# Kernel tuning notes

Measured on AMD Instinct MI355X. Metric: run time of the kernel, lower is better.

Reference implementation:

```python
import jax, jax.numpy as jnp
import numpy as np

B, DZ, DS, DH = 8192, 1024, 64, 4096

def setup_inputs() -> dict:
    key = jax.random.key(0)
    ks = jax.random.split(key, 8)
    r1 = 1.0 / np.sqrt(DZ)   # W1 init range (last dim dz)
    r2 = 1.0 / np.sqrt(DH)   # W2 init range (last dim dim_hidden)
    rc = 1.0 / np.sqrt(DS)   # C init range
    return {
        "z": jax.random.normal(ks[0], (B, DZ), jnp.float32),
        "s": jax.random.normal(ks[1], (B, DS), jnp.float32),
        "A": jnp.full((DZ,), 0.95, jnp.float32),
        "W1": jax.random.uniform(ks[2], (DH, DZ), jnp.float32, -r1, r1),
        "W2": jax.random.uniform(ks[3], (DZ, DH), jnp.float32, -r2, r2),
        "h1": jax.random.normal(ks[4], (DH,), jnp.float32),
        "h2": jax.random.normal(ks[5], (DZ,), jnp.float32),
        "C": jax.random.uniform(ks[6], (DZ, DS), jnp.float32, -rc, rc),
    }

def reference(z, s, A, W1, W2, h1, h2, C):
    # PLRNN step, W_trial=False, mean_center=False, noise=0:
    # z' = A*z + relu(z @ W1.T + h1) @ W2.T + h2 + s @ C.T
    z_activated = jax.nn.relu(z @ W1.T + h1)          # [B, DH]
    return A * z + z_activated @ W2.T + h2 + s @ C.T  # [B, DZ]
```

## Files before the change

kernel.cpp:

```cpp
#include <hip/hip_runtime.h>

#define BB 8192
#define DZ 1024
#define DS 64
#define DH 4096
#define KEXT (DH + DS)

typedef float floatx4 __attribute__((ext_vector_type(4)));
typedef __bf16 bf16x8 __attribute__((ext_vector_type(8)));
typedef __attribute__((address_space(1))) void* as1_void_ptr;
typedef __attribute__((address_space(3))) void* as3_void_ptr;

__device__ __forceinline__ void async_copy16(const void* g, void* l) {
    __builtin_amdgcn_global_load_lds((as1_void_ptr)g, (as3_void_ptr)l, 16, 0, 0);
}


__global__ void cvt_f32_bf16(const float* __restrict__ in, __bf16* __restrict__ out, int n4) {
    int i = blockIdx.x * blockDim.x + threadIdx.x;
    if (i < n4) {
        float4 v = ((const float4*)in)[i];
        __bf16* o = out + (size_t)i * 4;
        o[0] = (__bf16)v.x; o[1] = (__bf16)v.y; o[2] = (__bf16)v.z; o[3] = (__bf16)v.w;
    }
}

__global__ void build_B2(const float* __restrict__ W2, const float* __restrict__ C,
                         __bf16* __restrict__ B2b) {
    int j = blockIdx.x;
    for (int h = threadIdx.x; h < KEXT; h += 256) {
        float v = (h < DH) ? W2[(size_t)j * DH + h] : C[(size_t)j * DS + (h - DH)];
        B2b[(size_t)j * KEXT + h] = (__bf16)v;
    }
}

__global__ void stage_s(const float* __restrict__ s, __bf16* __restrict__ Hb) {
    int idx = blockIdx.x * 256 + threadIdx.x;
    int b = idx >> 6, k = idx & 63;
    Hb[(size_t)b * KEXT + DH + k] = (__bf16)s[idx];
}


__global__ __launch_bounds__(256) void gemm1_relu(
    const __bf16* __restrict__ Ag, const __bf16* __restrict__ Bg,
    const float* __restrict__ h1, __bf16* __restrict__ Hb)
{
    constexpr int K = DZ, ldA = DZ, ldB = DZ;
    __shared__ __align__(16) __bf16 As[128 * 32];
    __shared__ __align__(16) __bf16 Bs[128 * 32];

    const int tid = threadIdx.x;
    const int wave = tid >> 6, lane = tid & 63;
    const int wm = wave >> 1, wn = wave & 1;
    const int row0 = blockIdx.x * 128;
    const int col0 = blockIdx.y * 128;

    const __bf16* a0 = Ag + (size_t)(row0 + (tid >> 2)) * ldA + (tid & 3) * 8;
    const __bf16* b0 = Bg + (size_t)(col0 + (tid >> 2)) * ldB + (tid & 3) * 8;
    __bf16* lA = As + wave * 512;
    __bf16* lB = Bs + wave * 512;

    const __bf16* Afrag = As + (wm * 64 + (lane & 15)) * 32 + (lane >> 4) * 8;
    const __bf16* Bfrag = Bs + (wn * 64 + (lane & 15)) * 32 + (lane >> 4) * 8;

    floatx4 acc[4][4];
#pragma unroll
    for (int i = 0; i < 4; ++i)
#pragma unroll
        for (int j = 0; j < 4; ++j) acc[i][j] = (floatx4)0.0f;

    for (int kt = 0; kt < K / 32; ++kt) {
        const __bf16* ak = a0 + kt * 32;
        const __bf16* bk = b0 + kt * 32;
        async_copy16(ak,            lA);
        async_copy16(ak + 64 * ldA, lA + 2048);
        async_copy16(bk,            lB);
        async_copy16(bk + 64 * ldB, lB + 2048);
        __builtin_amdgcn_s_waitcnt(0);
        __syncthreads();

        bf16x8 af[4], bfr[4];
#pragma unroll
        for (int i = 0; i < 4; ++i) af[i] = *(const bf16x8*)(Afrag + i * 16 * 32);
#pragma unroll
        for (int j = 0; j < 4; ++j) bfr[j] = *(const bf16x8*)(Bfrag + j * 16 * 32);
#pragma unroll
        for (int i = 0; i < 4; ++i)
#pragma unroll
            for (int j = 0; j < 4; ++j)
                acc[i][j] = __builtin_amdgcn_mfma_f32_16x16x32_bf16(af[i], bfr[j], acc[i][j], 0, 0, 0);
        __syncthreads();
    }

    const int r0 = row0 + wm * 64 + (lane >> 4) * 4;
    const int c0 = col0 + wn * 64 + (lane & 15);
#pragma unroll
    for (int i = 0; i < 4; ++i) {
#pragma unroll
        for (int j = 0; j < 4; ++j) {
            int c = c0 + j * 16;
            float bias = h1[c];
#pragma unroll
            for (int rg = 0; rg < 4; ++rg) {
                int r = r0 + i * 16 + rg;
                float v = acc[i][j][rg] + bias;
                v = v > 0.0f ? v : 0.0f;
                Hb[(size_t)r * KEXT + c] = (__bf16)v;
            }
        }
    }
}


__global__ __launch_bounds__(256) void gemm2_out(
    const __bf16* __restrict__ Ag, const __bf16* __restrict__ Bg,
    const float* __restrict__ Adiag, const float* __restrict__ h2,
    const float* __restrict__ zf, float* __restrict__ out)
{
    constexpr int K = KEXT, ldA = KEXT, ldB = KEXT;
    __shared__ __align__(16) __bf16 As[128 * 32];
    __shared__ __align__(16) __bf16 Bs[128 * 32];

    const int tid = threadIdx.x;
    const int wave = tid >> 6, lane = tid & 63;
    const int wm = wave >> 1, wn = wave & 1;
    const int row0 = blockIdx.x * 128;
    const int col0 = blockIdx.y * 128;

    const __bf16* a0 = Ag + (size_t)(row0 + (tid >> 2)) * ldA + (tid & 3) * 8;
    const __bf16* b0 = Bg + (size_t)(col0 + (tid >> 2)) * ldB + (tid & 3) * 8;
    __bf16* lA = As + wave * 512;
    __bf16* lB = Bs + wave * 512;

    const __bf16* Afrag = As + (wm * 64 + (lane & 15)) * 32 + (lane >> 4) * 8;
    const __bf16* Bfrag = Bs + (wn * 64 + (lane & 15)) * 32 + (lane >> 4) * 8;

    floatx4 acc[4][4];
#pragma unroll
    for (int i = 0; i < 4; ++i)
#pragma unroll
        for (int j = 0; j < 4; ++j) acc[i][j] = (floatx4)0.0f;

    for (int kt = 0; kt < K / 32; ++kt) {
        const __bf16* ak = a0 + kt * 32;
        const __bf16* bk = b0 + kt * 32;
        async_copy16(ak,            lA);
        async_copy16(ak + 64 * ldA, lA + 2048);
        async_copy16(bk,            lB);
        async_copy16(bk + 64 * ldB, lB + 2048);
        __builtin_amdgcn_s_waitcnt(0);
        __syncthreads();

        bf16x8 af[4], bfr[4];
#pragma unroll
        for (int i = 0; i < 4; ++i) af[i] = *(const bf16x8*)(Afrag + i * 16 * 32);
#pragma unroll
        for (int j = 0; j < 4; ++j) bfr[j] = *(const bf16x8*)(Bfrag + j * 16 * 32);
#pragma unroll
        for (int i = 0; i < 4; ++i)
#pragma unroll
            for (int j = 0; j < 4; ++j)
                acc[i][j] = __builtin_amdgcn_mfma_f32_16x16x32_bf16(af[i], bfr[j], acc[i][j], 0, 0, 0);
        __syncthreads();
    }

    const int r0 = row0 + wm * 64 + (lane >> 4) * 4;
    const int c0 = col0 + wn * 64 + (lane & 15);
#pragma unroll
    for (int i = 0; i < 4; ++i) {
#pragma unroll
        for (int j = 0; j < 4; ++j) {
            int c = c0 + j * 16;
            float aj = Adiag[c];
            float hj = h2[c];
#pragma unroll
            for (int rg = 0; rg < 4; ++rg) {
                int r = r0 + i * 16 + rg;
                out[(size_t)r * DZ + c] = acc[i][j][rg] + aj * zf[(size_t)r * DZ + c] + hj;
            }
        }
    }
}


extern "C" void kernel_launch(void* const* d_in, const int* in_sizes, int n_in,
                              void* d_out, int out_size, void* d_ws, size_t ws_size,
                              hipStream_t stream) {
    const float* z  = (const float*)d_in[0];
    const float* s  = (const float*)d_in[1];
    const float* A  = (const float*)d_in[2];
    const float* W1 = (const float*)d_in[3];
    const float* W2 = (const float*)d_in[4];
    const float* h1 = (const float*)d_in[5];
    const float* h2 = (const float*)d_in[6];
    const float* C  = (const float*)d_in[7];
    float* out = (float*)d_out;

    char* ws = (char*)d_ws;
    size_t offHb  = 0;
    size_t offZb  = offHb  + (size_t)BB * KEXT * 2;
    size_t offW1b = offZb  + (size_t)BB * DZ * 2;
    size_t offB2b = offW1b + (size_t)DH * DZ * 2;
    __bf16* Hb  = (__bf16*)(ws + offHb);
    __bf16* zb  = (__bf16*)(ws + offZb);
    __bf16* W1b = (__bf16*)(ws + offW1b);
    __bf16* B2b = (__bf16*)(ws + offB2b);

    cvt_f32_bf16<<<(BB * DZ / 4 + 255) / 256, 256, 0, stream>>>(z, zb, BB * DZ / 4);
    cvt_f32_bf16<<<(DH * DZ / 4 + 255) / 256, 256, 0, stream>>>(W1, W1b, DH * DZ / 4);
    build_B2<<<DZ, 256, 0, stream>>>(W2, C, B2b);
    stage_s<<<BB * DS / 256, 256, 0, stream>>>(s, Hb);

    gemm1_relu<<<dim3(BB / 128, DH / 128), 256, 0, stream>>>(zb, W1b, h1, Hb);
    gemm2_out<<<dim3(BB / 128, DZ / 128), 256, 0, stream>>>(Hb, B2b, A, h2, z, out);
}
```

Measured before the change: 294.6 us.

## Stage GEMM1 epilogue via LDS and shrink GEMM2 tile to 64 rows

GEMM1's epilogue now writes bias+ReLU results into shared memory and then stores them to the hidden buffer as 16-byte coalesced rows, replacing scattered 2-byte stores. GEMM2 switches from 128x128 to 64x128 tiles with each wave owning 32 columns, doubling the grid (1024 blocks) to improve CU occupancy and balance. GEMM2's residual now reads the bf16 copy of z instead of fp32, halving that read at the cost of precision in the A*z term. The smaller GEMM2 tile lowers reuse per loaded byte and puts fewer MFMAs between barriers.

```diff
diff --git a/kernel.cpp b/kernel.cpp
--- a/kernel.cpp
+++ b/kernel.cpp
@@ -46,8 +46,9 @@
     const float* __restrict__ h1, __bf16* __restrict__ Hb)
 {
     constexpr int K = DZ, ldA = DZ, ldB = DZ;
-    __shared__ __align__(16) __bf16 As[128 * 32];
-    __shared__ __align__(16) __bf16 Bs[128 * 32];
+    __shared__ __align__(16) __bf16 smem[2 * 128 * 32];
+    __bf16* As = smem;
+    __bf16* Bs = smem + 128 * 32;
 
     const int tid = threadIdx.x;
     const int wave = tid >> 6, lane = tid & 63;
@@ -92,21 +93,41 @@
         __syncthreads();
     }
 
-    const int r0 = row0 + wm * 64 + (lane >> 4) * 4;
-    const int c0 = col0 + wn * 64 + (lane & 15);
-#pragma unroll
-    for (int i = 0; i < 4; ++i) {
-#pragma unroll
-        for (int j = 0; j < 4; ++j) {
-            int c = c0 + j * 16;
-            float bias = h1[c];
-#pragma unroll
-            for (int rg = 0; rg < 4; ++rg) {
-                int r = r0 + i * 16 + rg;
-                float v = acc[i][j][rg] + bias;
-                v = v > 0.0f ? v : 0.0f;
-                Hb[(size_t)r * KEXT + c] = (__bf16)v;
+    const int c_m = lane & 15;
+    const int q   = lane >> 4;
+    float bias[4];
+#pragma unroll
+    for (int j = 0; j < 4; ++j) bias[j] = h1[col0 + wn * 64 + c_m + j * 16];
+
+    constexpr int CST = 136;
+#pragma unroll
+    for (int p = 0; p < 4; ++p) {
+        __syncthreads();
+        if (wm == (p >> 1)) {
+#pragma unroll
+            for (int ii = 0; ii < 2; ++ii) {
+                const int i = (p & 1) * 2 + ii;
+#pragma unroll
+                for (int j = 0; j < 4; ++j) {
+                    const int c_l = wn * 64 + c_m + j * 16;
+#pragma unroll
+                    for (int rg = 0; rg < 4; ++rg) {
+                        const int r_l = q * 4 + ii * 16 + rg;
+                        float v = acc[i][j][rg] + bias[j];
+                        v = v > 0.0f ? v : 0.0f;
+                        smem[r_l * CST + c_l] = (__bf16)v;
+                    }
+                }
             }
+        }
+        __syncthreads();
+        const int rbase = row0 + p * 32;
+#pragma unroll
+        for (int it = 0; it < 2; ++it) {
+            const int idx = it * 256 + tid;
+            const int rr = idx >> 4, cc = (idx & 15) * 8;
+            *(bf16x8*)(Hb + (size_t)(rbase + rr) * KEXT + col0 + cc) =
+                *(const bf16x8*)(smem + rr * CST + cc);
         }
     }
 }
@@ -115,16 +136,15 @@
 __global__ __launch_bounds__(256) void gemm2_out(
     const __bf16* __restrict__ Ag, const __bf16* __restrict__ Bg,
     const float* __restrict__ Adiag, const float* __restrict__ h2,
-    const float* __restrict__ zf, float* __restrict__ out)
+    const __bf16* __restrict__ zb, float* __restrict__ out)
 {
     constexpr int K = KEXT, ldA = KEXT, ldB = KEXT;
-    __shared__ __align__(16) __bf16 As[128 * 32];
+    __shared__ __align__(16) __bf16 As[64 * 32];
     __shared__ __align__(16) __bf16 Bs[128 * 32];
 
     const int tid = threadIdx.x;
     const int wave = tid >> 6, lane = tid & 63;
-    const int wm = wave >> 1, wn = wave & 1;
-    const int row0 = blockIdx.x * 128;
+    const int row0 = blockIdx.x * 64;
     const int col0 = blockIdx.y * 128;
 
     const __bf16* a0 = Ag + (size_t)(row0 + (tid >> 2)) * ldA + (tid & 3) * 8;
@@ -132,51 +152,51 @@
     __bf16* lA = As + wave * 512;
     __bf16* lB = Bs + wave * 512;
 
-    const __bf16* Afrag = As + (wm * 64 + (lane & 15)) * 32 + (lane >> 4) * 8;
-    const __bf16* Bfrag = Bs + (wn * 64 + (lane & 15)) * 32 + (lane >> 4) * 8;
-
-    floatx4 acc[4][4];
+    const __bf16* Afrag = As + (lane & 15) * 32 + (lane >> 4) * 8;
+    const __bf16* Bfrag = Bs + (wave * 32 + (lane & 15)) * 32 + (lane >> 4) * 8;
+
+    floatx4 acc[4][2];
 #pragma unroll
     for (int i = 0; i < 4; ++i)
 #pragma unroll
-        for (int j = 0; j < 4; ++j) acc[i][j] = (floatx4)0.0f;
+        for (int j = 0; j < 2; ++j) acc[i][j] = (floatx4)0.0f;
 
     for (int kt = 0; kt < K / 32; ++kt) {
         const __bf16* ak = a0 + kt * 32;
         const __bf16* bk = b0 + kt * 32;
         async_copy16(ak,            lA);
-        async_copy16(ak + 64 * ldA, lA + 2048);
         async_copy16(bk,            lB);
         async_copy16(bk + 64 * ldB, lB + 2048);
         __builtin_amdgcn_s_waitcnt(0);
         __syncthreads();
 
-        bf16x8 af[4], bfr[4];
+        bf16x8 af[4], bfr[2];
 #pragma unroll
         for (int i = 0; i < 4; ++i) af[i] = *(const bf16x8*)(Afrag + i * 16 * 32);
 #pragma unroll
-        for (int j = 0; j < 4; ++j) bfr[j] = *(const bf16x8*)(Bfrag + j * 16 * 32);
+        for (int j = 0; j < 2; ++j) bfr[j] = *(const bf16x8*)(Bfrag + j * 16 * 32);
 #pragma unroll
         for (int i = 0; i < 4; ++i)
 #pragma unroll
-            for (int j = 0; j < 4; ++j)
+            for (int j = 0; j < 2; ++j)
                 acc[i][j] = __builtin_amdgcn_mfma_f32_16x16x32_bf16(af[i], bfr[j], acc[i][j], 0, 0, 0);
         __syncthreads();
     }
 
-    const int r0 = row0 + wm * 64 + (lane >> 4) * 4;
-    const int c0 = col0 + wn * 64 + (lane & 15);
+    const int r0 = row0 + (lane >> 4) * 4;
+    const int c0 = col0 + wave * 32 + (lane & 15);
 #pragma unroll
     for (int i = 0; i < 4; ++i) {
 #pragma unroll
-        for (int j = 0; j < 4; ++j) {
-            int c = c0 + j * 16;
-            float aj = Adiag[c];
-            float hj = h2[c];
+        for (int j = 0; j < 2; ++j) {
+            const int c = c0 + j * 16;
+            const float aj = Adiag[c];
+            const float hj = h2[c];
 #pragma unroll
             for (int rg = 0; rg < 4; ++rg) {
-                int r = r0 + i * 16 + rg;
-                out[(size_t)r * DZ + c] = acc[i][j][rg] + aj * zf[(size_t)r * DZ + c] + hj;
+                const int r = r0 + i * 16 + rg;
+                out[(size_t)r * DZ + c] =
+                    acc[i][j][rg] + aj * (float)zb[(size_t)r * DZ + c] + hj;
             }
         }
     }
@@ -212,5 +232,5 @@
     stage_s<<<BB * DS / 256, 256, 0, stream>>>(s, Hb);
 
     gemm1_relu<<<dim3(BB / 128, DH / 128), 256, 0, stream>>>(zb, W1b, h1, Hb);
-    gemm2_out<<<dim3(BB / 128, DZ / 128), 256, 0, stream>>>(Hb, B2b, A, h2, z, out);
-}
+    gemm2_out<<<dim3(BB / 64, DZ / 128), 256, 0, stream>>>(Hb, B2b, A, h2, zb, out);
+}
```

After: 309.2 us. 1.05x slower.
